# Performance work log

Hardware: AMD Instinct MI355X
Metric: run time of the kernel (lower is better)

## Reference

```python
import jax, jax.numpy as jnp
import numpy as np

N = 100000      # total nodes
E = 800000      # directed edges
DIN = 256       # input feature dim
H = 128         # hidden dim
EPS = 1e-5      # BatchNorm eps


def setup_inputs() -> dict:
    key = jax.random.key(0)
    ks = jax.random.split(key, 18)
    s = 0.05
    return {
        "x": jax.random.normal(ks[0], (N, DIN), jnp.float32),
        "src": jax.random.randint(ks[1], (E,), 0, N, dtype=jnp.int32),
        "dst": jax.random.randint(ks[2], (E,), 0, N, dtype=jnp.int32),
        "W1": jax.random.normal(ks[3], (DIN, H), jnp.float32) * s,
        "b1": jnp.zeros((H,), jnp.float32),
        "g1": jnp.ones((H,), jnp.float32),
        "be1": jnp.zeros((H,), jnp.float32),
        "W2": jax.random.normal(ks[4], (H, H), jnp.float32) * s,
        "b2": jnp.zeros((H,), jnp.float32),
        "g2": jnp.ones((H,), jnp.float32),
        "be2": jnp.zeros((H,), jnp.float32),
        "W3": jax.random.normal(ks[5], (H, H), jnp.float32) * s,
        "b3": jnp.zeros((H,), jnp.float32),
        "g3": jnp.ones((H,), jnp.float32),
        "be3": jnp.zeros((H,), jnp.float32),
        "Wf": jax.random.normal(ks[6], (H, 1), jnp.float32) * s,
        "bf": jnp.zeros((1,), jnp.float32),
    }


def _gcn_conv(h, W, b, src, dst, dis):
    # GCNConv: project, then sym-normalized aggregation over edges + self-loops
    h = h @ W                                   # [N, out]
    coef = dis[src] * dis[dst]                  # [E] edge norm weights
    agg = jax.ops.segment_sum(h[src] * coef[:, None], dst, num_segments=N)
    agg = agg + h * (dis * dis)[:, None]        # self-loop term (norm = 1/deg)
    return agg + b


def _bn_relu(h, g, be):
    # BatchNorm1d in training mode (batch stats over nodes, biased variance)
    mu = jnp.mean(h, axis=0)
    var = jnp.var(h, axis=0)
    return jax.nn.relu((h - mu) * (g / jnp.sqrt(var + EPS)) + be)


def reference(x, src, dst, W1, b1, g1, be1, W2, b2, g2, be2,
              W3, b3, g3, be3, Wf, bf):
    # degree of (A + I) counted on destination nodes, edge weight 1
    deg = jax.ops.segment_sum(jnp.ones((E,), jnp.float32), dst, num_segments=N) + 1.0
    dis = jax.lax.rsqrt(deg)                    # deg >= 1, safe

    h = _bn_relu(_gcn_conv(x, W1, b1, src, dst, dis), g1, be1)
    h = _bn_relu(_gcn_conv(h, W2, b2, src, dst, dis), g2, be2)
    h = _bn_relu(_gcn_conv(h, W3, b3, src, dst, dis), g3, be3)
    return h @ Wf + bf                          # [N, 1]
```

## Files before the change

kernel.cpp:

```cpp
#include <hip/hip_runtime.h>
#include <hip/hip_bf16.h>

typedef unsigned short ushort_t;
typedef __bf16 bf16x8 __attribute__((ext_vector_type(8)));
typedef unsigned short ushort8 __attribute__((ext_vector_type(8)));
typedef unsigned short ushort4v __attribute__((ext_vector_type(4)));
typedef float f32x4 __attribute__((ext_vector_type(4)));

#define HH 128
#define EPS 1e-5f
#define STAT_SLICES 32

__device__ __forceinline__ float bf2f(ushort_t u) {
    unsigned v = ((unsigned)u) << 16;
    return __builtin_bit_cast(float, v);
}
__device__ __forceinline__ ushort_t f2bf(float f) {
    unsigned u = __builtin_bit_cast(unsigned, f);
    unsigned r = (u + 0x7fffu + ((u >> 16) & 1u)) >> 16;
    return (ushort_t)r;
}
__device__ __forceinline__ float cvt(const void* p, int i, int flag) {
    return flag ? bf2f(((const ushort_t*)p)[i]) : ((const float*)p)[i];
}

__global__ void preK(const int* __restrict__ dst, int* __restrict__ counts, int E,
                     const void* W1, ushort_t* Wt1, const void* W2, ushort_t* Wt2,
                     const void* W3, ushort_t* Wt3,
                     const void* g1, const void* b1, const void* b2, const void* b3,
                     const void* g2, const void* g3, const void* be1, const void* be2,
                     const void* be3, const void* Wfp, const void* bfp,
                     float* __restrict__ cvec, int histB) {
    const int bid = blockIdx.x;
    const int tid = threadIdx.x;
    const int flag = (((const ushort_t*)g1)[0] == 0x3F80) ? 1 : 0;
    if (bid < histB) {
        int e = bid * 256 + tid;
        if (e < E) atomicAdd(&counts[dst[e]], 1);
    } else if (bid < histB + 256) {
        int idx = (bid - histB) * 256 + tid;
        const void* W; ushort_t* Wt; int Kp;
        if (idx < 32768)      { W = W1; Wt = Wt1; Kp = 264; }
        else if (idx < 49152) { W = W2; Wt = Wt2; Kp = 136; idx -= 32768; }
        else                  { W = W3; Wt = Wt3; Kp = 136; idx -= 49152; }
        int k = idx >> 7, nn = idx & 127;
        Wt[nn * Kp + k] = flag ? ((const ushort_t*)W)[idx] : f2bf(((const float*)W)[idx]);
    } else {
        int t = tid;
        if (t < 128) {
            cvec[t]        = cvt(b1, t, flag);
            cvec[128 + t]  = cvt(b2, t, flag);
            cvec[256 + t]  = cvt(b3, t, flag);
            cvec[384 + t]  = cvt(g1, t, flag);
            cvec[512 + t]  = cvt(g2, t, flag);
            cvec[640 + t]  = cvt(g3, t, flag);
            cvec[768 + t]  = cvt(be1, t, flag);
            cvec[896 + t]  = cvt(be2, t, flag);
            cvec[1024 + t] = cvt(be3, t, flag);
            cvec[1152 + t] = cvt(Wfp, t, flag);
            if (t == 0) cvec[1280] = cvt(bfp, 0, flag);
        }
    }
}

__global__ void scanAdisK(const int* __restrict__ cnt, int* __restrict__ partial,
                          float* __restrict__ dis, int n, int nbScan) {
    __shared__ int lds[256];
    const int tid = threadIdx.x;
    if ((int)blockIdx.x < nbScan) {
        int base = blockIdx.x * 2048 + tid * 8;
        int s = 0;
#pragma unroll
        for (int j = 0; j < 8; ++j) { int idx = base + j; if (idx < n) s += cnt[idx]; }
        lds[tid] = s; __syncthreads();
        for (int off = 128; off; off >>= 1) { if (tid < off) lds[tid] += lds[tid + off]; __syncthreads(); }
        if (tid == 0) partial[blockIdx.x] = lds[0];
    } else {
        int i = (blockIdx.x - nbScan) * 256 + tid;
        if (i < n) dis[i] = rsqrtf((float)cnt[i] + 1.0f);
    }
}

__global__ void scanB(int* __restrict__ partial, int* __restrict__ rowptr, int nb, int n) {
    if (threadIdx.x == 0) {
        int running = 0;
        for (int i = 0; i < nb; ++i) { int v = partial[i]; partial[i] = running; running += v; }
        rowptr[n] = running;
    }
}

__device__ __forceinline__ void scanCDev(int* lds, const int* __restrict__ cnt,
                                         const int* __restrict__ partial,
                                         int* __restrict__ rowptr, int n, int bid) {
    const int tid = threadIdx.x;
    int base = bid * 2048 + tid * 8;
    int v[8]; int s = 0;
#pragma unroll
    for (int j = 0; j < 8; ++j) { int idx = base + j; v[j] = (idx < n) ? cnt[idx] : 0; s += v[j]; }
    lds[tid] = s; __syncthreads();
    for (int off = 1; off < 256; off <<= 1) {
        int x = (tid >= off) ? lds[tid - off] : 0;
        __syncthreads();
        lds[tid] += x;
        __syncthreads();
    }
    int excl = lds[tid] - s;
    int off0 = partial[bid] + excl;
#pragma unroll
    for (int j = 0; j < 8; ++j) {
        int idx = base + j;
        if (idx < n) { rowptr[idx] = off0; off0 += v[j]; }
    }
}

__global__ void scatterK(const int* __restrict__ src, const int* __restrict__ dst,
                         const int* __restrict__ rowptr, int* __restrict__ fill,
                         const float* __restrict__ dis,
                         uint2* __restrict__ erec, int E) {
    int e = blockIdx.x * 256 + threadIdx.x;
    if (e >= E) return;
    int d = dst[e], s = src[e];
    int old = atomicSub(&fill[d], 1);
    int pos = rowptr[d] + old - 1;
    float c = dis[s] * dis[d];
    uint2 r; r.x = (unsigned)s; r.y = __builtin_bit_cast(unsigned, c);
    erec[pos] = r;
}

template <bool BN, bool EXT, int K>
__device__ __forceinline__ void mmDev(char* smemRaw, const void* __restrict__ Av,
                                      const ushort_t* __restrict__ Wt,
                                      ushort_t* __restrict__ out, int n,
                                      const float* __restrict__ ssum,
                                      const float* __restrict__ ssq,
                                      const float* __restrict__ gam,
                                      const float* __restrict__ bet,
                                      const ushort_t* __restrict__ flagRef, int bid) {
    constexpr int KP  = K + 8;
    constexpr int BKP = 136;
    constexpr int NCH = K / 128;
    constexpr int NST = K / 32;

    ushort_t* bs = (ushort_t*)smemRaw;
    float* scw = (float*)(smemRaw + 128 * BKP * 2);

    const int tid  = threadIdx.x;
    const int lane = tid & 63;
    const int wave = tid >> 6;
    const int m = lane & 15;
    const int q = lane >> 4;

    if constexpr (BN) {
        if (tid < 128) {
            float S = 0.f, Q = 0.f;
#pragma unroll
            for (int sl = 0; sl < STAT_SLICES; ++sl) { S += ssum[sl * HH + tid]; Q += ssq[sl * HH + tid]; }
            float invn = 1.0f / (float)n;
            float mu = S * invn;
            float var = fmaxf(Q * invn - mu * mu, 0.f);
            float sc = gam[tid] * rsqrtf(var + EPS);
            scw[tid] = sc;
            scw[128 + tid] = bet[tid] - mu * sc;
        }
        __syncthreads();
    }

    const int flag = EXT ? ((flagRef[0] == 0x3F80) ? 1 : 0) : 1;

    int rowA = bid * 64 + wave * 16 + m;
    int rA = rowA < n ? rowA : (n - 1);

    ushort8 a[NST];
    if (EXT && !flag) {
        const float* ap32 = (const float*)Av + (size_t)rA * K + q * 8;
#pragma unroll
        for (int s = 0; s < NST; ++s) {
            float4 f0 = *(const float4*)(ap32 + s * 32);
            float4 f1 = *(const float4*)(ap32 + s * 32 + 4);
            a[s][0] = f2bf(f0.x); a[s][1] = f2bf(f0.y); a[s][2] = f2bf(f0.z); a[s][3] = f2bf(f0.w);
            a[s][4] = f2bf(f1.x); a[s][5] = f2bf(f1.y); a[s][6] = f2bf(f1.z); a[s][7] = f2bf(f1.w);
        }
    } else {
        const ushort_t* ap16 = (const ushort_t*)Av + (size_t)rA * K + q * 8;
#pragma unroll
        for (int s = 0; s < NST; ++s) a[s] = *(const ushort8*)(ap16 + s * 32);
    }
    if constexpr (BN) {
#pragma unroll
        for (int s = 0; s < NST; ++s) {
            int kb = s * 32 + q * 8;
#pragma unroll
            for (int j = 0; j < 8; ++j) {
                float f = fmaxf(bf2f(a[s][j]) * scw[kb + j] + scw[128 + kb + j], 0.f);
                a[s][j] = f2bf(f);
            }
        }
    }

    f32x4 acc[8];
#pragma unroll
    for (int t = 0; t < 8; ++t) acc[t] = (f32x4){0.f, 0.f, 0.f, 0.f};

#pragma unroll
    for (int c = 0; c < NCH; ++c) {
#pragma unroll
        for (int r = 0; r < 8; ++r) {
            int idx = tid + r * 256;
            int row = idx >> 4, seg = idx & 15;
            *(uint4*)&bs[row * BKP + seg * 8] =
                *(const uint4*)&Wt[(size_t)row * KP + c * 128 + seg * 8];
        }
        __syncthreads();
#pragma unroll
        for (int s = 0; s < 4; ++s) {
            bf16x8 nf = __builtin_bit_cast(bf16x8, a[c * 4 + s]);
#pragma unroll
            for (int t = 0; t < 8; ++t) {
                ushort8 wv = *(const ushort8*)&bs[(t * 16 + m) * BKP + s * 32 + q * 8];
                acc[t] = __builtin_amdgcn_mfma_f32_16x16x32_bf16(
                    __builtin_bit_cast(bf16x8, wv), nf, acc[t], 0, 0, 0);
            }
        }
        if (c + 1 < NCH) __syncthreads();
    }

    const int node_g = bid * 64 + wave * 16 + m;
    if (node_g < n) {
        ushort_t* op = out + (size_t)node_g * HH + q * 4;
#pragma unroll
        for (int t = 0; t < 8; ++t) {
            ushort4v pk;
#pragma unroll
            for (int r = 0; r < 4; ++r) pk[r] = f2bf(acc[t][r]);
            *(ushort4v*)(op + t * 16) = pk;
        }
    }
}

__global__ __launch_bounds__(256) void mm1scanCK(const void* __restrict__ x,
                                                 const ushort_t* __restrict__ Wt1,
                                                 ushort_t* __restrict__ tbuf, int n,
                                                 const ushort_t* __restrict__ flagRef,
                                                 const int* __restrict__ cnt,
                                                 const int* __restrict__ partial,
                                                 int* __restrict__ rowptr, int mmB) {
    __shared__ char smem[35840];
    if ((int)blockIdx.x < mmB)
        mmDev<false, true, 256>(smem, x, Wt1, tbuf, n, nullptr, nullptr, nullptr, nullptr,
                                flagRef, blockIdx.x);
    else
        scanCDev((int*)smem, cnt, partial, rowptr, n, blockIdx.x - mmB);
}

template <int K>
__global__ __launch_bounds__(256) void mmBNK(const ushort_t* __restrict__ A,
                                             const ushort_t* __restrict__ Wt,
                                             ushort_t* __restrict__ out, int n,
                                             const float* __restrict__ ssum,
                                             const float* __restrict__ ssq,
                                             const float* __restrict__ gam,
                                             const float* __restrict__ bet) {
    __shared__ char smem[35840];
    mmDev<true, false, K>(smem, A, Wt, out, n, ssum, ssq, gam, bet, nullptr, blockIdx.x);
}

__global__ __launch_bounds__(256) void aggK(const ushort_t* __restrict__ t,
                                            const uint2* __restrict__ erec,
                                            const int* __restrict__ rowptr,
                                            const float* __restrict__ dis,
                                            const float* __restrict__ bias,
                                            ushort_t* __restrict__ g,
                                            float* __restrict__ ssum, float* __restrict__ ssq,
                                            int n) {
    const int lane = threadIdx.x & 63;
    const int wave = threadIdx.x >> 6;
    const int cb = lane * 2;
    const float b0 = bias[cb], b1 = bias[cb + 1];
    float s0 = 0.f, s1 = 0.f, q0 = 0.f, q1 = 0.f;

    for (int node = blockIdx.x * 4 + wave; node < n; node += gridDim.x * 4) {
        float d = dis[node];
        float d2 = d * d;
        unsigned sv = *(const unsigned*)(t + (size_t)node * HH + cb);
        float a0 = bf2f((ushort_t)(sv & 0xffff)) * d2;
        float a1 = bf2f((ushort_t)(sv >> 16)) * d2;

        int beg = rowptr[node], end = rowptr[node + 1];
        for (int eb = beg; eb < end; eb += 64) {
            int rem = end - eb; if (rem > 64) rem = 64;
            uint2 rec = (lane < rem) ? erec[eb + lane] : (uint2){0u, 0u};
            int es = (int)rec.x;
            float ec = __builtin_bit_cast(float, rec.y);
            int rr = (rem + 7) & ~7;
            for (int j = 0; j < rr; j += 8) {
                int ii[8]; float cc[8]; unsigned ww[8];
#pragma unroll
                for (int k = 0; k < 8; ++k) {
                    ii[k] = __shfl(es, j + k);
                    cc[k] = __shfl(ec, j + k);
                }
#pragma unroll
                for (int k = 0; k < 8; ++k)
                    ww[k] = *(const unsigned*)(t + (size_t)ii[k] * HH + cb);
#pragma unroll
                for (int k = 0; k < 8; ++k) {
                    a0 += bf2f((ushort_t)(ww[k] & 0xffff)) * cc[k];
                    a1 += bf2f((ushort_t)(ww[k] >> 16)) * cc[k];
                }
            }
        }
        a0 += b0; a1 += b1;
        unsigned packed = (unsigned)f2bf(a0) | ((unsigned)f2bf(a1) << 16);
        *(unsigned*)(g + (size_t)node * HH + cb) = packed;
        s0 += a0; s1 += a1; q0 += a0 * a0; q1 += a1 * a1;
    }

    __shared__ float red[4][64][4];
    red[wave][lane][0] = s0; red[wave][lane][1] = s1;
    red[wave][lane][2] = q0; red[wave][lane][3] = q1;
    __syncthreads();
    if (wave == 0) {
        float S0 = 0, S1 = 0, Q0 = 0, Q1 = 0;
#pragma unroll
        for (int w = 0; w < 4; ++w) {
            S0 += red[w][lane][0]; S1 += red[w][lane][1];
            Q0 += red[w][lane][2]; Q1 += red[w][lane][3];
        }
        int slice = (blockIdx.x & (STAT_SLICES - 1)) * HH;
        atomicAdd(&ssum[slice + cb], S0);
        atomicAdd(&ssum[slice + cb + 1], S1);
        atomicAdd(&ssq[slice + cb], Q0);
        atomicAdd(&ssq[slice + cb + 1], Q1);
    }
}

__global__ __launch_bounds__(256) void outK(const ushort_t* __restrict__ g,
                                            const float* __restrict__ ssum,
                                            const float* __restrict__ ssq,
                                            const float* __restrict__ gam,
                                            const float* __restrict__ bet,
                                            const float* __restrict__ Wf,
                                            const float* __restrict__ bfp,
                                            void* __restrict__ outv, int n,
                                            const ushort_t* __restrict__ flagRef) {
    __shared__ float scw[256];
    const int tid = threadIdx.x;
    if (tid < 128) {
        float S = 0.f, Q = 0.f;
#pragma unroll
        for (int sl = 0; sl < STAT_SLICES; ++sl) { S += ssum[sl * HH + tid]; Q += ssq[sl * HH + tid]; }
        float invn = 1.0f / (float)n;
        float mu = S * invn;
        float var = fmaxf(Q * invn - mu * mu, 0.f);
        float sc = gam[tid] * rsqrtf(var + EPS);
        scw[tid] = sc;
        scw[128 + tid] = bet[tid] - mu * sc;
    }
    __syncthreads();

    const int lane = tid & 63;
    const int wave = tid >> 6;
    const int cb = lane * 2;
    const float w0 = Wf[cb], w1 = Wf[cb + 1];
    const float sc0 = scw[cb], sc1 = scw[cb + 1];
    const float sh0 = scw[128 + cb], sh1 = scw[128 + cb + 1];
    const float bb = bfp[0];
    const int flag = (flagRef[0] == 0x3F80) ? 1 : 0;

    for (int node = blockIdx.x * 4 + wave; node < n; node += gridDim.x * 4) {
        unsigned v = *(const unsigned*)(g + (size_t)node * HH + cb);
        float h0 = fmaxf(bf2f((ushort_t)(v & 0xffff)) * sc0 + sh0, 0.f);
        float h1 = fmaxf(bf2f((ushort_t)(v >> 16)) * sc1 + sh1, 0.f);
        float x = h0 * w0 + h1 * w1;
#pragma unroll
        for (int off = 32; off; off >>= 1) x += __shfl_down(x, off);
        if (lane == 0) {
            float r = x + bb;
            if (flag) ((ushort_t*)outv)[node] = f2bf(r);
            else      ((float*)outv)[node] = r;
        }
    }
}

extern "C" void kernel_launch(void* const* d_in, const int* in_sizes, int n_in,
                              void* d_out, int out_size, void* d_ws, size_t ws_size,
                              hipStream_t stream) {
    const int DIN = 256;
    const int N = in_sizes[0] / DIN;
    const int E = in_sizes[1];

    const void* x   = d_in[0];
    const int*  src = (const int*)d_in[1];
    const int*  dst = (const int*)d_in[2];
    const void* W1  = d_in[3];
    const void* b1  = d_in[4];
    const void* g1  = d_in[5];
    const void* be1 = d_in[6];
    const void* W2  = d_in[7];
    const void* b2  = d_in[8];
    const void* g2  = d_in[9];
    const void* be2 = d_in[10];
    const void* W3  = d_in[11];
    const void* b3  = d_in[12];
    const void* g3  = d_in[13];
    const void* be3 = d_in[14];
    const void* Wf  = d_in[15];
    const void* bfp = d_in[16];
    const ushort_t* flagRef = (const ushort_t*)g1;

    char* base = (char*)d_ws;
    size_t off = 0;
    auto carve = [&](size_t bytes) -> void* {
        void* p = base + off;
        off += (bytes + 255) & ~(size_t)255;
        return p;
    };
    int*      counts = (int*)carve((size_t)N * 4);
    float*    stats  = (float*)carve((size_t)3 * 2 * STAT_SLICES * HH * 4);
    size_t    zbytes = off;
    float*    dis    = (float*)carve((size_t)N * 4);
    int*      rowptr = (int*)carve((size_t)(N + 1) * 4);
    int*      partial= (int*)carve(256 * 4);
    uint2*    erec   = (uint2*)carve((size_t)E * 8);
    ushort_t* Wt1    = (ushort_t*)carve((size_t)128 * 264 * 2);
    ushort_t* Wt2    = (ushort_t*)carve((size_t)128 * 136 * 2);
    ushort_t* Wt3    = (ushort_t*)carve((size_t)128 * 136 * 2);
    ushort_t* tbuf   = (ushort_t*)carve((size_t)N * HH * 2);
    ushort_t* gbuf   = (ushort_t*)carve((size_t)N * HH * 2);
    float*    cvec   = (float*)carve((size_t)1281 * 4);

    float* ssum0 = stats;                         float* ssq0 = ssum0 + STAT_SLICES * HH;
    float* ssum1 = ssq0 + STAT_SLICES * HH;       float* ssq1 = ssum1 + STAT_SLICES * HH;
    float* ssum2 = ssq1 + STAT_SLICES * HH;       float* ssq2 = ssum2 + STAT_SLICES * HH;

    float* c_b1 = cvec;         float* c_b2 = cvec + 128;  float* c_b3 = cvec + 256;
    float* c_g1 = cvec + 384;   float* c_g2 = cvec + 512;  float* c_g3 = cvec + 640;
    float* c_be1 = cvec + 768;  float* c_be2 = cvec + 896; float* c_be3 = cvec + 1024;
    float* c_Wf = cvec + 1152;  float* c_bf = cvec + 1280;

    const int nbScan = (N + 2047) / 2048;
    const int histB  = (E + 255) / 256;
    const int disB   = (N + 255) / 256;
    const int mmB    = (N + 63) / 64;
    const int aggB   = 2048;

    hipMemsetAsync(d_ws, 0, zbytes, stream);

    preK<<<histB + 256 + 1, 256, 0, stream>>>(dst, counts, E, W1, Wt1, W2, Wt2, W3, Wt3,
                                              g1, b1, b2, b3, g2, g3, be1, be2, be3, Wf, bfp,
                                              cvec, histB);
    scanAdisK<<<nbScan + disB, 256, 0, stream>>>(counts, partial, dis, N, nbScan);
    scanB<<<1, 64, 0, stream>>>(partial, rowptr, nbScan, N);
    mm1scanCK<<<mmB + nbScan, 256, 0, stream>>>(x, Wt1, tbuf, N, flagRef,
                                                counts, partial, rowptr, mmB);
    scatterK<<<histB, 256, 0, stream>>>(src, dst, rowptr, counts, dis, erec, E);

    aggK<<<aggB, 256, 0, stream>>>(tbuf, erec, rowptr, dis, c_b1, gbuf, ssum0, ssq0, N);
    mmBNK<128><<<mmB, 256, 0, stream>>>(gbuf, Wt2, tbuf, N, ssum0, ssq0, c_g1, c_be1);
    aggK<<<aggB, 256, 0, stream>>>(tbuf, erec, rowptr, dis, c_b2, gbuf, ssum1, ssq1, N);
    mmBNK<128><<<mmB, 256, 0, stream>>>(gbuf, Wt3, tbuf, N, ssum1, ssq1, c_g2, c_be2);
    aggK<<<aggB, 256, 0, stream>>>(tbuf, erec, rowptr, dis, c_b3, gbuf, ssum2, ssq2, N);
    outK<<<1024, 256, 0, stream>>>(gbuf, ssum2, ssq2, c_g3, c_be3, c_Wf, c_bf, d_out, N, flagRef);
}
```

Baseline: 459.5 us.

## Make GEMM kernels persistent with resident swizzled weights and prefetched A tiles

The first-layer and BN-fused GEMM kernels become persistent grids (512 and 1024 blocks). Each block loads the whole transposed weight matrix into LDS once, using an XOR swizzle instead of padding, then loops over row tiles while prefetching the next tile's activations into registers. The separate single-thread scanB launch is removed: each scan block now sums the block partials itself. The aim is to cut repeated weight staging, per-tile barriers and one kernel launch, at the cost of larger LDS use (64 KB for layer 1), which lowers occupancy, and more register pressure from the double-buffered A fragments.

```diff
diff --git a/kernel.cpp b/kernel.cpp
--- a/kernel.cpp
+++ b/kernel.cpp
@@ -10,6 +10,8 @@
 #define HH 128
 #define EPS 1e-5f
 #define STAT_SLICES 32
+#define MM1_GRID 512
+#define MMBN_GRID 1024
 
 __device__ __forceinline__ float bf2f(ushort_t u) {
     unsigned v = ((unsigned)u) << 16;
@@ -39,12 +41,12 @@
         if (e < E) atomicAdd(&counts[dst[e]], 1);
     } else if (bid < histB + 256) {
         int idx = (bid - histB) * 256 + tid;
-        const void* W; ushort_t* Wt; int Kp;
-        if (idx < 32768)      { W = W1; Wt = Wt1; Kp = 264; }
-        else if (idx < 49152) { W = W2; Wt = Wt2; Kp = 136; idx -= 32768; }
-        else                  { W = W3; Wt = Wt3; Kp = 136; idx -= 49152; }
+        const void* W; ushort_t* Wt; int K;
+        if (idx < 32768)      { W = W1; Wt = Wt1; K = 256; }
+        else if (idx < 49152) { W = W2; Wt = Wt2; K = 128; idx -= 32768; }
+        else                  { W = W3; Wt = Wt3; K = 128; idx -= 49152; }
         int k = idx >> 7, nn = idx & 127;
-        Wt[nn * Kp + k] = flag ? ((const ushort_t*)W)[idx] : f2bf(((const float*)W)[idx]);
+        Wt[nn * K + k] = flag ? ((const ushort_t*)W)[idx] : f2bf(((const float*)W)[idx]);
     } else {
         int t = tid;
         if (t < 128) {
@@ -81,18 +83,12 @@
     }
 }
 
-__global__ void scanB(int* __restrict__ partial, int* __restrict__ rowptr, int nb, int n) {
-    if (threadIdx.x == 0) {
-        int running = 0;
-        for (int i = 0; i < nb; ++i) { int v = partial[i]; partial[i] = running; running += v; }
-        rowptr[n] = running;
-    }
-}
-
-__device__ __forceinline__ void scanCDev(int* lds, const int* __restrict__ cnt,
-                                         const int* __restrict__ partial,
-                                         int* __restrict__ rowptr, int n, int bid) {
-    const int tid = threadIdx.x;
+__device__ __forceinline__ void scanC2Dev(int* lds, const int* __restrict__ cnt,
+                                          const int* __restrict__ partial,
+                                          int* __restrict__ rowptr, int n, int bid, int nb) {
+    const int tid = threadIdx.x;
+    int pre = 0, tot = 0;
+    for (int i = 0; i < nb; ++i) { int v = partial[i]; if (i < bid) pre += v; tot += v; }
     int base = bid * 2048 + tid * 8;
     int v[8]; int s = 0;
 #pragma unroll
@@ -105,12 +101,13 @@
         __syncthreads();
     }
     int excl = lds[tid] - s;
-    int off0 = partial[bid] + excl;
+    int off0 = pre + excl;
 #pragma unroll
     for (int j = 0; j < 8; ++j) {
         int idx = base + j;
         if (idx < n) { rowptr[idx] = off0; off0 += v[j]; }
     }
+    if (bid == 0 && tid == 0) rowptr[n] = tot;
 }
 
 __global__ void scatterK(const int* __restrict__ src, const int* __restrict__ dst,
@@ -127,132 +124,91 @@
     erec[pos] = r;
 }
 
-template <bool BN, bool EXT, int K>
-__device__ __forceinline__ void mmDev(char* smemRaw, const void* __restrict__ Av,
-                                      const ushort_t* __restrict__ Wt,
-                                      ushort_t* __restrict__ out, int n,
-                                      const float* __restrict__ ssum,
-                                      const float* __restrict__ ssq,
-                                      const float* __restrict__ gam,
-                                      const float* __restrict__ bet,
-                                      const ushort_t* __restrict__ flagRef, int bid) {
-    constexpr int KP  = K + 8;
-    constexpr int BKP = 136;
-    constexpr int NCH = K / 128;
-    constexpr int NST = K / 32;
-
-    ushort_t* bs = (ushort_t*)smemRaw;
-    float* scw = (float*)(smemRaw + 128 * BKP * 2);
-
-    const int tid  = threadIdx.x;
-    const int lane = tid & 63;
-    const int wave = tid >> 6;
-    const int m = lane & 15;
-    const int q = lane >> 4;
-
-    if constexpr (BN) {
-        if (tid < 128) {
-            float S = 0.f, Q = 0.f;
-#pragma unroll
-            for (int sl = 0; sl < STAT_SLICES; ++sl) { S += ssum[sl * HH + tid]; Q += ssq[sl * HH + tid]; }
-            float invn = 1.0f / (float)n;
-            float mu = S * invn;
-            float var = fmaxf(Q * invn - mu * mu, 0.f);
-            float sc = gam[tid] * rsqrtf(var + EPS);
-            scw[tid] = sc;
-            scw[128 + tid] = bet[tid] - mu * sc;
-        }
-        __syncthreads();
-    }
-
-    const int flag = EXT ? ((flagRef[0] == 0x3F80) ? 1 : 0) : 1;
-
-    int rowA = bid * 64 + wave * 16 + m;
-    int rA = rowA < n ? rowA : (n - 1);
-
-    ushort8 a[NST];
-    if (EXT && !flag) {
-        const float* ap32 = (const float*)Av + (size_t)rA * K + q * 8;
-#pragma unroll
-        for (int s = 0; s < NST; ++s) {
-            float4 f0 = *(const float4*)(ap32 + s * 32);
-            float4 f1 = *(const float4*)(ap32 + s * 32 + 4);
-            a[s][0] = f2bf(f0.x); a[s][1] = f2bf(f0.y); a[s][2] = f2bf(f0.z); a[s][3] = f2bf(f0.w);
-            a[s][4] = f2bf(f1.x); a[s][5] = f2bf(f1.y); a[s][6] = f2bf(f1.z); a[s][7] = f2bf(f1.w);
-        }
-    } else {
-        const ushort_t* ap16 = (const ushort_t*)Av + (size_t)rA * K + q * 8;
-#pragma unroll
-        for (int s = 0; s < NST; ++s) a[s] = *(const ushort8*)(ap16 + s * 32);
-    }
-    if constexpr (BN) {
-#pragma unroll
-        for (int s = 0; s < NST; ++s) {
-            int kb = s * 32 + q * 8;
-#pragma unroll
-            for (int j = 0; j < 8; ++j) {
-                float f = fmaxf(bf2f(a[s][j]) * scw[kb + j] + scw[128 + kb + j], 0.f);
-                a[s][j] = f2bf(f);
-            }
-        }
-    }
-
-    f32x4 acc[8];
-#pragma unroll
-    for (int t = 0; t < 8; ++t) acc[t] = (f32x4){0.f, 0.f, 0.f, 0.f};
-
-#pragma unroll
-    for (int c = 0; c < NCH; ++c) {
-#pragma unroll
-        for (int r = 0; r < 8; ++r) {
-            int idx = tid + r * 256;
-            int row = idx >> 4, seg = idx & 15;
-            *(uint4*)&bs[row * BKP + seg * 8] =
-                *(const uint4*)&Wt[(size_t)row * KP + c * 128 + seg * 8];
-        }
-        __syncthreads();
-#pragma unroll
-        for (int s = 0; s < 4; ++s) {
-            bf16x8 nf = __builtin_bit_cast(bf16x8, a[c * 4 + s]);
-#pragma unroll
-            for (int t = 0; t < 8; ++t) {
-                ushort8 wv = *(const ushort8*)&bs[(t * 16 + m) * BKP + s * 32 + q * 8];
-                acc[t] = __builtin_amdgcn_mfma_f32_16x16x32_bf16(
-                    __builtin_bit_cast(bf16x8, wv), nf, acc[t], 0, 0, 0);
-            }
-        }
-        if (c + 1 < NCH) __syncthreads();
-    }
-
-    const int node_g = bid * 64 + wave * 16 + m;
-    if (node_g < n) {
-        ushort_t* op = out + (size_t)node_g * HH + q * 4;
-#pragma unroll
-        for (int t = 0; t < 8; ++t) {
-            ushort4v pk;
-#pragma unroll
-            for (int r = 0; r < 4; ++r) pk[r] = f2bf(acc[t][r]);
-            *(ushort4v*)(op + t * 16) = pk;
-        }
-    }
-}
-
 __global__ __launch_bounds__(256) void mm1scanCK(const void* __restrict__ x,
                                                  const ushort_t* __restrict__ Wt1,
                                                  ushort_t* __restrict__ tbuf, int n,
                                                  const ushort_t* __restrict__ flagRef,
                                                  const int* __restrict__ cnt,
                                                  const int* __restrict__ partial,
-                                                 int* __restrict__ rowptr, int mmB) {
-    __shared__ char smem[35840];
-    if ((int)blockIdx.x < mmB)
-        mmDev<false, true, 256>(smem, x, Wt1, tbuf, n, nullptr, nullptr, nullptr, nullptr,
-                                flagRef, blockIdx.x);
-    else
-        scanCDev((int*)smem, cnt, partial, rowptr, n, blockIdx.x - mmB);
-}
-
-template <int K>
+                                                 int* __restrict__ rowptr, int nbScan) {
+    __shared__ char smem[65536];
+    const int tid = threadIdx.x;
+    if ((int)blockIdx.x < nbScan) {
+        scanC2Dev((int*)smem, cnt, partial, rowptr, n, blockIdx.x, nbScan);
+        return;
+    }
+    const int bid = blockIdx.x - nbScan;
+
+#pragma unroll
+    for (int it = 0; it < 16; ++it) {
+        int idx = tid + it * 256;
+        int row = idx >> 5, seg = idx & 31;
+        int p = seg ^ (row & 7);
+        *(uint4*)&smem[row * 512 + p * 16] = *(const uint4*)&Wt1[row * 256 + seg * 8];
+    }
+    __syncthreads();
+
+    const int lane = tid & 63, wave = tid >> 6;
+    const int m = lane & 15, q = lane >> 4;
+    const int flag = (flagRef[0] == 0x3F80) ? 1 : 0;
+    const int nTiles = (n + 63) >> 6;
+
+    auto loadA = [&](int tile, ushort8* a) {
+        int r = tile * 64 + wave * 16 + m;
+        if (r >= n) r = n - 1;
+        if (flag) {
+            const ushort_t* p0 = (const ushort_t*)x + (size_t)r * 256 + q * 8;
+#pragma unroll
+            for (int s = 0; s < 8; ++s) a[s] = *(const ushort8*)(p0 + s * 32);
+        } else {
+            const float* p0 = (const float*)x + (size_t)r * 256 + q * 8;
+#pragma unroll
+            for (int s = 0; s < 8; ++s) {
+                float4 f0 = *(const float4*)(p0 + s * 32);
+                float4 f1 = *(const float4*)(p0 + s * 32 + 4);
+                a[s][0] = f2bf(f0.x); a[s][1] = f2bf(f0.y); a[s][2] = f2bf(f0.z); a[s][3] = f2bf(f0.w);
+                a[s][4] = f2bf(f1.x); a[s][5] = f2bf(f1.y); a[s][6] = f2bf(f1.z); a[s][7] = f2bf(f1.w);
+            }
+        }
+    };
+
+    ushort8 cur[8], nxt[8];
+    int tile = bid;
+    if (tile < nTiles) loadA(tile, cur);
+    for (; tile < nTiles; tile += MM1_GRID) {
+        int tnext = tile + MM1_GRID;
+        if (tnext < nTiles) loadA(tnext, nxt);
+
+        f32x4 acc[8];
+#pragma unroll
+        for (int t = 0; t < 8; ++t) acc[t] = (f32x4){0.f, 0.f, 0.f, 0.f};
+#pragma unroll
+        for (int s = 0; s < 8; ++s) {
+            bf16x8 nf = __builtin_bit_cast(bf16x8, cur[s]);
+#pragma unroll
+            for (int t = 0; t < 8; ++t) {
+                int p = (s * 4 + q) ^ (m & 7);
+                ushort8 wv = *(const ushort8*)&smem[(t * 16 + m) * 512 + p * 16];
+                acc[t] = __builtin_amdgcn_mfma_f32_16x16x32_bf16(
+                    __builtin_bit_cast(bf16x8, wv), nf, acc[t], 0, 0, 0);
+            }
+        }
+        int node_g = tile * 64 + wave * 16 + m;
+        if (node_g < n) {
+            ushort_t* op = tbuf + (size_t)node_g * HH + q * 4;
+#pragma unroll
+            for (int t = 0; t < 8; ++t) {
+                ushort4v pk;
+#pragma unroll
+                for (int r = 0; r < 4; ++r) pk[r] = f2bf(acc[t][r]);
+                *(ushort4v*)(op + t * 16) = pk;
+            }
+        }
+#pragma unroll
+        for (int s = 0; s < 8; ++s) cur[s] = nxt[s];
+    }
+}
+
 __global__ __launch_bounds__(256) void mmBNK(const ushort_t* __restrict__ A,
                                              const ushort_t* __restrict__ Wt,
                                              ushort_t* __restrict__ out, int n,
@@ -260,8 +216,85 @@
                                              const float* __restrict__ ssq,
                                              const float* __restrict__ gam,
                                              const float* __restrict__ bet) {
-    __shared__ char smem[35840];
-    mmDev<true, false, K>(smem, A, Wt, out, n, ssum, ssq, gam, bet, nullptr, blockIdx.x);
+    __shared__ char smem[33792];
+    float* scw = (float*)(smem + 32768);
+    const int tid = threadIdx.x;
+
+    if (tid < 128) {
+        float S = 0.f, Q = 0.f;
+#pragma unroll
+        for (int sl = 0; sl < STAT_SLICES; ++sl) { S += ssum[sl * HH + tid]; Q += ssq[sl * HH + tid]; }
+        float invn = 1.0f / (float)n;
+        float mu = S * invn;
+        float var = fmaxf(Q * invn - mu * mu, 0.f);
+        float sc = gam[tid] * rsqrtf(var + EPS);
+        scw[tid] = sc;
+        scw[128 + tid] = bet[tid] - mu * sc;
+    }
+#pragma unroll
+    for (int it = 0; it < 8; ++it) {
+        int idx = tid + it * 256;
+        int row = idx >> 4, seg = idx & 15;
+        int p = seg ^ (row & 7);
+        *(uint4*)&smem[row * 256 + p * 16] = *(const uint4*)&Wt[row * 128 + seg * 8];
+    }
+    __syncthreads();
+
+    const int lane = tid & 63, wave = tid >> 6;
+    const int m = lane & 15, q = lane >> 4;
+    const int nTiles = (n + 63) >> 6;
+
+    auto loadA = [&](int tile, ushort8* a) {
+        int r = tile * 64 + wave * 16 + m;
+        if (r >= n) r = n - 1;
+        const ushort_t* p0 = A + (size_t)r * 128 + q * 8;
+#pragma unroll
+        for (int s = 0; s < 4; ++s) a[s] = *(const ushort8*)(p0 + s * 32);
+    };
+
+    ushort8 cur[4], nxt[4];
+    int tile = blockIdx.x;
+    if (tile < nTiles) loadA(tile, cur);
+    for (; tile < nTiles; tile += MMBN_GRID) {
+        int tnext = tile + MMBN_GRID;
+        if (tnext < nTiles) loadA(tnext, nxt);
+
+#pragma unroll
+        for (int s = 0; s < 4; ++s) {
+            int kb = s * 32 + q * 8;
+#pragma unroll
+            for (int j = 0; j < 8; ++j)
+                cur[s][j] = f2bf(fmaxf(bf2f(cur[s][j]) * scw[kb + j] + scw[128 + kb + j], 0.f));
+        }
+
+        f32x4 acc[8];
+#pragma unroll
+        for (int t = 0; t < 8; ++t) acc[t] = (f32x4){0.f, 0.f, 0.f, 0.f};
+#pragma unroll
+        for (int s = 0; s < 4; ++s) {
+            bf16x8 nf = __builtin_bit_cast(bf16x8, cur[s]);
+#pragma unroll
+            for (int t = 0; t < 8; ++t) {
+                int p = (s * 4 + q) ^ (m & 7);
+                ushort8 wv = *(const ushort8*)&smem[(t * 16 + m) * 256 + p * 16];
+                acc[t] = __builtin_amdgcn_mfma_f32_16x16x32_bf16(
+                    __builtin_bit_cast(bf16x8, wv), nf, acc[t], 0, 0, 0);
+            }
+        }
+        int node_g = tile * 64 + wave * 16 + m;
+        if (node_g < n) {
+            ushort_t* op = out + (size_t)node_g * HH + q * 4;
+#pragma unroll
+            for (int t = 0; t < 8; ++t) {
+                ushort4v pk;
+#pragma unroll
+                for (int r = 0; r < 4; ++r) pk[r] = f2bf(acc[t][r]);
+                *(ushort4v*)(op + t * 16) = pk;
+            }
+        }
+#pragma unroll
+        for (int s = 0; s < 4; ++s) cur[s] = nxt[s];
+    }
 }
 
 __global__ __launch_bounds__(256) void aggK(const ushort_t* __restrict__ t,
@@ -422,9 +455,9 @@
     int*      rowptr = (int*)carve((size_t)(N + 1) * 4);
     int*      partial= (int*)carve(256 * 4);
     uint2*    erec   = (uint2*)carve((size_t)E * 8);
-    ushort_t* Wt1    = (ushort_t*)carve((size_t)128 * 264 * 2);
-    ushort_t* Wt2    = (ushort_t*)carve((size_t)128 * 136 * 2);
-    ushort_t* Wt3    = (ushort_t*)carve((size_t)128 * 136 * 2);
+    ushort_t* Wt1    = (ushort_t*)carve((size_t)128 * 256 * 2);
+    ushort_t* Wt2    = (ushort_t*)carve((size_t)128 * 128 * 2);
+    ushort_t* Wt3    = (ushort_t*)carve((size_t)128 * 128 * 2);
     ushort_t* tbuf   = (ushort_t*)carve((size_t)N * HH * 2);
     ushort_t* gbuf   = (ushort_t*)carve((size_t)N * HH * 2);
     float*    cvec   = (float*)carve((size_t)1281 * 4);
@@ -441,7 +474,6 @@
     const int nbScan = (N + 2047) / 2048;
     const int histB  = (E + 255) / 256;
     const int disB   = (N + 255) / 256;
-    const int mmB    = (N + 63) / 64;
     const int aggB   = 2048;
 
     hipMemsetAsync(d_ws, 0, zbytes, stream);
@@ -450,15 +482,14 @@
                                               g1, b1, b2, b3, g2, g3, be1, be2, be3, Wf, bfp,
                                               cvec, histB);
     scanAdisK<<<nbScan + disB, 256, 0, stream>>>(counts, partial, dis, N, nbScan);
-    scanB<<<1, 64, 0, stream>>>(partial, rowptr, nbScan, N);
-    mm1scanCK<<<mmB + nbScan, 256, 0, stream>>>(x, Wt1, tbuf, N, flagRef,
-                                                counts, partial, rowptr, mmB);
+    mm1scanCK<<<nbScan + MM1_GRID, 256, 0, stream>>>(x, Wt1, tbuf, N, flagRef,
+                                                     counts, partial, rowptr, nbScan);
     scatterK<<<histB, 256, 0, stream>>>(src, dst, rowptr, counts, dis, erec, E);
 
     aggK<<<aggB, 256, 0, stream>>>(tbuf, erec, rowptr, dis, c_b1, gbuf, ssum0, ssq0, N);
-    mmBNK<128><<<mmB, 256, 0, stream>>>(gbuf, Wt2, tbuf, N, ssum0, ssq0, c_g1, c_be1);
+    mmBNK<<<MMBN_GRID, 256, 0, stream>>>(gbuf, Wt2, tbuf, N, ssum0, ssq0, c_g1, c_be1);
     aggK<<<aggB, 256, 0, stream>>>(tbuf, erec, rowptr, dis, c_b2, gbuf, ssum1, ssq1, N);
-    mmBNK<128><<<mmB, 256, 0, stream>>>(gbuf, Wt3, tbuf, N, ssum1, ssq1, c_g2, c_be2);
+    mmBNK<<<MMBN_GRID, 256, 0, stream>>>(gbuf, Wt3, tbuf, N, ssum1, ssq1, c_g2, c_be2);
     aggK<<<aggB, 256, 0, stream>>>(tbuf, erec, rowptr, dis, c_b3, gbuf, ssum2, ssq2, N);
     outK<<<1024, 256, 0, stream>>>(gbuf, ssum2, ssq2, c_g3, c_be3, c_Wf, c_bf, d_out, N, flagRef);
 }
```

Result: no change. 452.9 us (-1.4%).
